# Kernel optimization log

Measured on AMD Instinct MI355X. Metric: run time of the kernel, lower is better.

Reference implementation:

```python
import jax, jax.numpy as jnp
import numpy as np

ALPHA, NCLUST, LAMBD, GAMMA = 0.6, 3, 0.1, 0.01
KMEANS_ITERS = 10


def _conv(x, w, b):
    y = jax.lax.conv_general_dilated(x, w, (1, 1), 'SAME',
                                     dimension_numbers=('NCHW', 'OIHW', 'NCHW'))
    return y + b[None, :, None, None]


def _pool2(x):
    B, C, H, W = x.shape
    return x.reshape(B, C, H // 2, 2, W // 2, 2).mean(axis=(3, 5))


def _up2(x):
    return jnp.repeat(jnp.repeat(x, 2, axis=2), 2, axis=3)


def _encode(x, p, all_features=False):
    f1 = jax.nn.relu(_conv(x, p['e1_w'], p['e1_b']))
    f2 = jax.nn.relu(_conv(_pool2(f1), p['e2_w'], p['e2_b']))
    f3 = jax.nn.relu(_conv(_pool2(f2), p['e3_w'], p['e3_b']))
    f4 = jax.nn.relu(_conv(_pool2(f3), p['e4_w'], p['e4_b']))
    return (f1, f2, f3, f4) if all_features else f4


def _decode(f, p):
    x = jax.nn.relu(_conv(f, p['d1_w'], p['d1_b']))
    x = jax.nn.relu(_conv(_up2(x), p['d2_w'], p['d2_b']))
    x = jax.nn.relu(_conv(_up2(x), p['d3_w'], p['d3_b']))
    return _conv(_up2(x), p['d4_w'], p['d4_b'])


def _kmeans_onehot(pts, k):
    # pts: [N, C]; fixed-iteration Lloyd's, init = first k points.
    cent0 = pts[:k]

    def step(cent, _):
        d = ((pts[:, None, :] - cent[None]) ** 2).sum(-1)  # [N, K]
        oh = jax.nn.one_hot(jnp.argmin(d, axis=1), k, dtype=pts.dtype)
        cent = (oh.T @ pts) / (oh.sum(0)[:, None] + 1e-6)
        return cent, None

    cent, _ = jax.lax.scan(step, cent0, None, length=KMEANS_ITERS)
    d = ((pts[:, None, :] - cent[None]) ** 2).sum(-1)
    return jax.nn.one_hot(jnp.argmin(d, axis=1), k, dtype=pts.dtype)  # [N, K]


def _style_transfer(fc, fs):
    # fc, fs: [C, H, W] single-sample encoded features (original runs this per-sample on CPU numpy).
    C, H, W = fc.shape
    f = fc.reshape(C, -1)  # [C, N]
    s = fs.reshape(C, -1)  # [C, M]
    oh_c = _kmeans_onehot(f.T, NCLUST)  # [N, K]
    oh_s = _kmeans_onehot(s.T, NCLUST)  # [M, K]
    eye = LAMBD * jnp.eye(C, dtype=f.dtype)

    def cluster_T(wc, ws):
        # weighted whitening-coloring transform for one cluster pair
        nc = wc.sum() + 1e-6
        ns = ws.sum() + 1e-6
        mu_c = (f * wc).sum(1) / nc
        mu_s = (s * ws).sum(1) / ns
        fc_ = f - mu_c[:, None]
        fs_ = s - mu_s[:, None]
        cov_c = (fc_ * wc) @ fc_.T / nc + eye
        cov_s = (fs_ * ws) @ fs_.T / ns + eye
        lc, Ec = jnp.linalg.eigh(cov_c)
        ls, Es = jnp.linalg.eigh(cov_s)
        Wm = (Ec * jnp.clip(lc, 1e-6) ** -0.5) @ Ec.T  # whiten
        Cm = (Es * jnp.clip(ls, 1e-6) ** 0.5) @ Es.T   # color
        return Cm @ Wm, mu_c, mu_s

    Ts, mucs, muss = jax.vmap(cluster_T, in_axes=(1, 1))(oh_c, oh_s)  # [K,C,C],[K,C],[K,C]
    tpts = (jnp.einsum('kcd,dn->kcn', Ts, f)
            - jnp.einsum('kcd,kd->kc', Ts, mucs)[:, :, None]
            + muss[:, :, None])  # [K, C, N]
    fcs = jnp.einsum('nk,kcn->cn', oh_c, tpts)  # select per-point cluster transform
    return (ALPHA * fcs + (1.0 - ALPHA) * f).reshape(C, H, W)


def _forward(content_images, style_images, p):
    cf = _encode(content_images, p)
    sf = _encode(style_images, p)
    # original detaches to numpy -> no grad through the transfer
    tf_ = jax.lax.stop_gradient(jax.vmap(_style_transfer)(cf, sf))
    dec = _decode(tf_, p)
    ef = _encode(dec, p)
    all_ef = _encode(dec, p, all_features=True)
    all_sf = _encode(style_images, p, all_features=True)
    closs = jnp.mean((ef - cf) ** 2)
    sloss = 0.0
    for fa, fb in zip(all_ef, all_sf):
        sloss = sloss + jnp.mean((fa.mean((2, 3)) - fb.mean((2, 3))) ** 2)
        sloss = sloss + jnp.mean((fa.std((2, 3)) - fb.std((2, 3))) ** 2)
    return closs + GAMMA * sloss


PARAM_SHAPES = dict(
    e1_w=(64, 3, 3, 3), e1_b=(64,), e2_w=(128, 64, 3, 3), e2_b=(128,),
    e3_w=(256, 128, 3, 3), e3_b=(256,), e4_w=(512, 256, 3, 3), e4_b=(512,),
    d1_w=(256, 512, 3, 3), d1_b=(256,), d2_w=(128, 256, 3, 3), d2_b=(128,),
    d3_w=(64, 128, 3, 3), d3_b=(64,), d4_w=(3, 64, 3, 3), d4_b=(3,),
)


def setup_inputs() -> dict:
    key = jax.random.key(0)
    kc, ks, kp = jax.random.split(key, 3)
    inp = {
        'content_images': jax.random.uniform(kc, (4, 3, 256, 256), jnp.float32),
        'style_images': jax.random.uniform(ks, (4, 3, 256, 256), jnp.float32),
    }
    for i, (name, shp) in enumerate(PARAM_SHAPES.items()):
        fan_in = int(np.prod(shp[1:])) if len(shp) > 1 else 1
        inp[name] = jax.random.normal(jax.random.fold_in(kp, i), shp, jnp.float32) / np.sqrt(fan_in)
    return inp


def reference(content_images, style_images, e1_w, e1_b, e2_w, e2_b, e3_w, e3_b,
              e4_w, e4_b, d1_w, d1_b, d2_w, d2_b, d3_w, d3_b, d4_w, d4_b):
    p = dict(e1_w=e1_w, e1_b=e1_b, e2_w=e2_w, e2_b=e2_b, e3_w=e3_w, e3_b=e3_b,
             e4_w=e4_w, e4_b=e4_b, d1_w=d1_w, d1_b=d1_b, d2_w=d2_w, d2_b=d2_b,
             d3_w=d3_w, d3_b=d3_b, d4_w=d4_w, d4_b=d4_b)
    return _forward(content_images, style_images, p)
```

## Files before the change

### kernel.cpp

```cpp
#include <hip/hip_runtime.h>
#include <cstddef>

#define NS_ITERS 8
#define MSZ 262144
#define PL  6291456
#define KSLOT 12312

typedef unsigned short u16;
typedef __attribute__((ext_vector_type(8))) short bf16x8;
typedef __attribute__((ext_vector_type(4))) float f32x4;
typedef __attribute__((ext_vector_type(4))) short u16x4;

__device__ inline u16 bf16_rne(float x){
  unsigned u = __float_as_uint(x);
  unsigned r = u + 0x7fffu + ((u>>16)&1u);
  return (u16)(r>>16);
}
__device__ inline float bf16f(u16 h){
  return __uint_as_float(((unsigned)h)<<16);
}

#define OFF_F4C   0ul
#define OFF_F4S   2097152ul
#define OFF_TF    4194304ul
// ... 217 lines not shown
      const int c = (gc<<3) + i;
      float v;
      if constexpr (POOL){
        const float* p = in + ((size_t)(b*C + c0+c)*(Ho*2) + ho*2)*(size_t)(Wo*2) + (size_t)wo*2;
        v = 0.25f*(p[0] + p[1] + p[2*Wo] + p[2*Wo+1]);
      } else {
        v = in[((size_t)(b*C + c0+c))*N + n];
      }
      u16 h = bf16_rne(v);
      tr[c][lnn] = (unsigned)h | ((unsigned)bf16_rne(v - bf16f(h)) << 16);
    }
  }
  __syncthreads();
  const int n2 = threadIdx.x >> 3, oct = threadIdx.x & 7;
  bf16x8 vh, vl;
  #pragma unroll
  for (int j=0;j<8;j++){
    unsigned u = tr[(oct<<3)+j][n2];
    vh[j] = (short)(u & 0xffffu);
    vl[j] = (short)(u >> 16);
  }
  size_t o = ((size_t)b*N + (n0 + n2))*(size_t)C + c0 + (oct<<3);
  *(bf16x8*)&oh[o] = vh;
  *(bf16x8*)&ol[o] = vl;
}

template<int KS, int RESIZE>
__global__ __launch_bounds__(256,4) void convm(
    const u16* __restrict__ xh, const u16* __restrict__ xl,
    const u16* __restrict__ wsh, const u16* __restrict__ wsl,
    const float* __restrict__ bias, float* __restrict__ out,
    int Cin, int Cout, int H, int W, int relu)
{
  const int tilesW = W >> 4;
  const int h0 = (blockIdx.x / tilesW) << 3;
  const int w0 = (blockIdx.x % tilesW) << 4;
  const int co0 = blockIdx.y << 6;
  const int b  = blockIdx.z / KS;
  const int ks = blockIdx.z % KS;
  const int NB = gridDim.z / KS;
  const int tid = threadIdx.x;
  const int wid = tid >> 6, lane = tid & 63;
  const int wm = wid >> 1, wn = wid & 1;
  const int quad = lane >> 4, ln = lane & 15;

  __shared__ __align__(16) u16 sXh[180*40], sXl[180*40];
  __shared__ __align__(16) u16 sWh[64*40],  sWl[64*40];

  f32x4 acc[2][4];
  #pragma unroll
  for (int i=0;i<2;i++)
    #pragma unroll
    for (int j=0;j<4;j++)
      #pragma unroll
      for (int e=0;e<4;e++) acc[i][j][e] = 0.f;

  const int wco = tid >> 2, wcg = (tid & 3) << 3;

  const int ciA = ks*(Cin/KS), ciB = ciA + Cin/KS;
  for (int ci0 = ciA; ci0 < ciB; ci0 += 32){
    for (int e = tid; e < 720; e += 256){
      const int px = e >> 2, sl = e & 3;
      const int pr = px / 18, pc = px - pr*18;
      const int ih = h0 + pr - 1, iw = w0 + pc - 1;
      bf16x8 vh, vl;
      #pragma unroll
      for (int j=0;j<8;j++){ vh[j] = 0; vl[j] = 0; }
      if ((unsigned)ih < (unsigned)H && (unsigned)iw < (unsigned)W){
        size_t o;
        if constexpr (RESIZE==0)
          o = ((size_t)(b*H + ih)*W + iw)*(size_t)Cin + (size_t)(ci0 + sl*8);
        else
          o = ((size_t)(b*(H>>1) + (ih>>1))*(W>>1) + (iw>>1))*(size_t)Cin + (size_t)(ci0 + sl*8);
        vh = *(const bf16x8*)&xh[o];
        vl = *(const bf16x8*)&xl[o];
      }
      *(bf16x8*)&sXh[px*40 + sl*8] = vh;
      *(bf16x8*)&sXl[px*40 + sl*8] = vl;
    }
    for (int dh = 0; dh < 3; ++dh){
      for (int dw = 0; dw < 3; ++dw){
        {
          const size_t so = ((size_t)((dh*3+dw)*Cout + co0+wco))*Cin + ci0 + wcg;
          *(bf16x8*)&sWh[wco*40 + wcg] = *(const bf16x8*)&wsh[so];
          *(bf16x8*)&sWl[wco*40 + wcg] = *(const bf16x8*)&wsl[so];
        }
        __syncthreads();
        bf16x8 ah[2], al[2], bh[4], bl[4];
        #pragma unroll
        for (int t=0;t<2;t++){
          const int co_l = (wm*2+t)*16 + ln;
          ah[t] = *(const bf16x8*)&sWh[co_l*40 + quad*8];
          al[t] = *(const bf16x8*)&sWl[co_l*40 + quad*8];
        }
        #pragma unroll
        for (int t=0;t<4;t++){
          const int p = (wn*4+t)*16 + ln;
          const int px = ((p>>4) + dh)*18 + (p&15) + dw;
          const int xo = px*40 + quad*8;
          bh[t] = *(const bf16x8*)&sXh[xo];
          bl[t] = *(const bf16x8*)&sXl[xo];
        }
        #pragma unroll
        for (int mi=0;mi<2;mi++)
          #pragma unroll
          for (int ni=0;ni<4;ni++){
            acc[mi][ni] = __builtin_amdgcn_mfma_f32_16x16x32_bf16(ah[mi], bh[ni], acc[mi][ni], 0, 0, 0);
            acc[mi][ni] = __builtin_amdgcn_mfma_f32_16x16x32_bf16(ah[mi], bl[ni], acc[mi][ni], 0, 0, 0);
            acc[mi][ni] = __builtin_amdgcn_mfma_f32_16x16x32_bf16(al[mi], bh[ni], acc[mi][ni], 0, 0, 0);
          }
        __syncthreads();
      }
    }
  }
  #pragma unroll
  for (int mi=0;mi<2;mi++){
    const int co = co0 + (wm*2+mi)*16 + quad*4;
    #pragma unroll
    for (int ni=0;ni<4;ni++){
      const int p = (wn*4+ni)*16 + ln;
      const int oh = h0 + (p>>4), ow = w0 + (p&15);
      #pragma unroll
      for (int rg=0; rg<4; rg++){
        const int cog = co + rg;
        if constexpr (KS==1){
          float v = acc[mi][ni][rg] + bias[cog];
          if (relu) v = fmaxf(v, 0.f);
          out[((size_t)(b*Cout + cog)*H + oh)*W + ow] = v;
        } else {
          out[((size_t)((ks*NB + b)*Cout + cog)*H + oh)*W + ow] = acc[mi][ni][rg];
        }
      }
    }
  }
}

__global__ __launch_bounds__(256) void sumk(const float* __restrict__ part, const float* __restrict__ bias,
                                            float* __restrict__ out, int Cout, int HW, int KS, int relu, int n){
  int idx = blockIdx.x*256 + threadIdx.x;
  if (idx >= n) return;
  int co = (idx / HW) % Cout;
  float v = bias[co];
  for (int k=0;k<KS;k++) v += part[(size_t)k*n + idx];
  if (relu) v = fmaxf(v, 0.f);
  out[idx] = v;
}

__global__ __launch_bounds__(256) void statsk(const float* __restrict__ x, int HW,
                                              float* __restrict__ mo, float* __restrict__ so){
  int bc = blockIdx.x, tid = threadIdx.x;
  const float* p = x + (size_t)bc*HW;
  double s = 0.0, s2 = 0.0;
  for (int i = tid; i < HW; i += 256){ double v = p[i]; s += v; s2 += v*v; }
  __shared__ double sh[256], sh2[256];
  sh[tid] = s; sh2[tid] = s2; __syncthreads();
  for (int k=128;k>0;k>>=1){ if (tid<k){ sh[tid]+=sh[tid+k]; sh2[tid]+=sh2[tid+k]; } __syncthreads(); }
  if (tid == 0){
    double m = sh[0]/HW;
    double var = sh2[0]/HW - m*m;
    if (var < 0.0) var = 0.0;
    mo[bc] = (float)m;
    so[bc] = (float)sqrt(var);
  }
}

__global__ __launch_bounds__(256) void transposek(const float* __restrict__ f4c,
                                                  const float* __restrict__ f4s,
                                                  float* __restrict__ ptsT){
  __shared__ float t[32][33];
  int r = blockIdx.z;
  const float* src = (r < 4) ? (f4c + (size_t)r*524288) : (f4s + (size_t)(r-4)*524288);
  int n0 = blockIdx.x*32, c0 = blockIdx.y*32;
  int lx = threadIdx.x & 31, ly = threadIdx.x >> 5;
  for (int j=0;j<32;j+=8)
    t[ly+j][lx] = src[(size_t)(c0+ly+j)*1024 + n0+lx];
  __syncthreads();
  for (int j=0;j<32;j+=8)
    ptsT[((size_t)r*1024 + n0+ly+j)*512 + c0+lx] = t[lx][ly+j];
}

__global__ __launch_bounds__(256) void initcent2k(const float* __restrict__ ptsT, float* __restrict__ KACC){
  int i = blockIdx.x*256 + threadIdx.x;
  if (i < 12288){
    int c = i & 511; int k = (i >> 9) % 3; int r = i / 1536;
    KACC[r*1536 + k*512 + c] = ptsT[((size_t)r*1024 + k)*512 + c];
  }
  if (i < 24) KACC[12288 + i] = 1.f;
}

__global__ __launch_bounds__(256) void kstepk(const float* __restrict__ ptsT,
    const float* __restrict__ prev, float* __restrict__ next,
    int* __restrict__ a, int nodiv)
{
  const int r = blockIdx.x, sl = blockIdx.y;
  const int tid = threadIdx.x;
  __shared__ float sc[1536];
  __shared__ int sa[32];
  __shared__ float red[3][8][32];
  __shared__ int scnt[3];
  if (tid < 3) scnt[tid] = 0;
  for (int i = tid; i < 1536; i += 256){
    float s = prev[r*1536 + i];
    float cnt = nodiv ? 1.f : (prev[12288 + r*3 + (i>>9)] + 1e-6f);
    sc[i] = s / cnt;
  }
  __syncthreads();
  const float* base = ptsT + (size_t)r*524288;
  const int wid = tid >> 6, lane = tid & 63;
  for (int rep = 0; rep < 8; ++rep){
    int p = wid*8 + rep;
    int n = sl*32 + p;
    const float* pp = base + (size_t)n*512;
    float d0=0.f,d1=0.f,d2=0.f;
    #pragma unroll
    for (int i=0;i<8;i++){
      int c = lane + i*64;
      float v = pp[c];
      float e0 = v - sc[c], e1 = v - sc[512+c], e2 = v - sc[1024+c];
      d0 = fmaf(e0,e0,d0); d1 = fmaf(e1,e1,d1); d2 = fmaf(e2,e2,d2);
    }
    #pragma unroll
    for (int off=32; off>0; off>>=1){
      d0 += __shfl_down(d0, off, 64);
      d1 += __shfl_down(d1, off, 64);
      d2 += __shfl_down(d2, off, 64);
    }
    if (lane == 0){
      int bi = 0; float bd = d0;
      if (d1 < bd){ bd = d1; bi = 1; }
      if (d2 < bd){ bd = d2; bi = 2; }
      sa[p] = bi;
      a[r*1024 + n] = bi;
    }
  }
  __syncthreads();
  if (tid < 32) atomicAdd(&scnt[sa[tid]], 1);
  __syncthreads();
  if (tid < 3) atomicAdd(&next[12288 + r*3 + tid], (float)scnt[tid]);
  const int g = tid >> 5, lc = tid & 31;
  for (int cj = 0; cj < 16; ++cj){
    int c = cj*32 + lc;
    float s0=0.f,s1=0.f,s2=0.f;
    #pragma unroll
    for (int q=0;q<4;q++){
      int nl = g*4 + q;
      float v = base[(size_t)(sl*32+nl)*512 + c];
      int an = sa[nl];
      s0 += (an==0)?v:0.f;
      s1 += (an==1)?v:0.f;
      s2 += (an==2)?v:0.f;
    }
    red[0][g][lc]=s0; red[1][g][lc]=s1; red[2][g][lc]=s2;
    __syncthreads();
    if (g == 0){
      float t0=0.f,t1=0.f,t2=0.f;
      #pragma unroll
      for (int q2=0;q2<8;q2++){ t0+=red[0][q2][lc]; t1+=red[1][q2][lc]; t2+=red[2][q2][lc]; }
      atomicAdd(&next[r*1536 +          c], t0);
      atomicAdd(&next[r*1536 +  512 +   c], t1);
      atomicAdd(&next[r*1536 + 1024 +   c], t2);
    }
    __syncthreads();
  }
}

__global__ __launch_bounds__(256) void mufink(const float* __restrict__ slot,
                                              float* __restrict__ mu, float* __restrict__ counts){
  int i = blockIdx.x*256 + threadIdx.x;
  if (i >= 12288) return;
  int c = i & 511; int k = (i >> 9) % 3; int r = i / 1536;
  int cs = r >> 2, img = r & 3;
  int i0 = cs*12 + img*3;
  float cnt = slot[12288 + r*3 + k];
  mu[(size_t)(i0+k)*512 + c] = slot[r*1536 + k*512 + c] / (cnt + 1e-6f);
  if (c == 0) counts[i0+k] = cnt;
}

__global__ __launch_bounds__(256) void maskcenterk(const float* __restrict__ f4c, const float* __restrict__ f4s,
        const int* __restrict__ a, const float* __restrict__ mu,
        u16* __restrict__ Ph, u16* __restrict__ Pl){
  size_t i4 = ((size_t)blockIdx.x*256 + threadIdx.x)*4;
  if (i4 >= (size_t)PL*2) return;
  int z = (int)(i4 >> 19);
  int rc = (int)(i4 & 524287);
  int c = rc >> 10, n = rc & 1023;
  int cs = z / 12; int rem = z - cs*12; int img = rem / 3; int k = rem - img*3;
  const float* pts = (cs ? f4s : f4c) + (size_t)img*524288;
  float m = mu[(size_t)z*512 + c];
  const int* an = a + (cs*4 + img)*1024 + n;
  float4 v4 = *(const float4*)&pts[(size_t)c*1024 + n];
  float vv[4] = {v4.x, v4.y, v4.z, v4.w};
  u16x4 oh, ol;
  #pragma unroll
  for (int j=0;j<4;j++){
    float v = (an[j] == k) ? (vv[j] - m) : 0.f;
    u16 h = bf16_rne(v);
    oh[j] = (short)h;
    ol[j] = (short)bf16_rne(v - bf16f(h));
  }
  *(u16x4*)&Ph[i4] = oh;
  *(u16x4*)&Pl[i4] = ol;
}

__global__ __launch_bounds__(256,4) void covgemm(const u16* __restrict__ Ph, const u16* __restrict__ Pl,
        const float* __restrict__ counts, float* __restrict__ Ycov, float* __restrict__ trsum){
  const int z = blockIdx.z;
  const u16* Pbh = Ph + (size_t)z*524288;
  const u16* Pbl = Pl + (size_t)z*524288;
  const int m0 = blockIdx.y*128, n0 = blockIdx.x*64;
  const int tid = threadIdx.x;

  __shared__ __align__(16) u16 sAh[128*40], sAl[128*40];
  __shared__ __align__(16) u16 sBh[64*40], sBl[64*40];

  const int ra = tid >> 2, qa = tid & 3;
  const int wid = tid >> 6, lane = tid & 63;
  const int wm = wid >> 1, wn = wid & 1;
  const int quad = lane >> 4, ln = lane & 15;

  f32x4 acc[4][2];
  #pragma unroll
  for (int i=0;i<4;i++)
    #pragma unroll
    for (int j=0;j<2;j++)
      #pragma unroll
      for (int e=0;e<4;e++) acc[i][j][e] = 0.f;

  for (int k0 = 0; k0 < 1024; k0 += 32){
    *(bf16x8*)&sAh[ra*40 + qa*8]      = *(const bf16x8*)&Pbh[(size_t)(m0+ra)*1024    + k0 + qa*8];
    *(bf16x8*)&sAl[ra*40 + qa*8]      = *(const bf16x8*)&Pbl[(size_t)(m0+ra)*1024    + k0 + qa*8];
    *(bf16x8*)&sAh[(ra+64)*40 + qa*8] = *(const bf16x8*)&Pbh[(size_t)(m0+ra+64)*1024 + k0 + qa*8];
    *(bf16x8*)&sAl[(ra+64)*40 + qa*8] = *(const bf16x8*)&Pbl[(size_t)(m0+ra+64)*1024 + k0 + qa*8];
    *(bf16x8*)&sBh[ra*40 + qa*8]      = *(const bf16x8*)&Pbh[(size_t)(n0+ra)*1024    + k0 + qa*8];
    *(bf16x8*)&sBl[ra*40 + qa*8]      = *(const bf16x8*)&Pbl[(size_t)(n0+ra)*1024    + k0 + qa*8];
    __syncthreads();

    bf16x8 ah[4], al[4], bh[2], bl[2];
    #pragma unroll
    for (int t=0;t<4;t++){
      const int moA = ((wm*4+t)*16 + ln)*40 + quad*8;
      ah[t] = *(const bf16x8*)&sAh[moA];
      al[t] = *(const bf16x8*)&sAl[moA];
    }
    #pragma unroll
    for (int t=0;t<2;t++){
      const int moB = ((wn*2+t)*16 + ln)*40 + quad*8;
      bh[t] = *(const bf16x8*)&sBh[moB];
      bl[t] = *(const bf16x8*)&sBl[moB];
    }
    #pragma unroll
    for (int mi=0;mi<4;mi++)
      #pragma unroll
      for (int ni=0;ni<2;ni++){
        acc[mi][ni] = __builtin_amdgcn_mfma_f32_16x16x32_bf16(ah[mi], bh[ni], acc[mi][ni], 0, 0, 0);
        acc[mi][ni] = __builtin_amdgcn_mfma_f32_16x16x32_bf16(ah[mi], bl[ni], acc[mi][ni], 0, 0, 0);
        acc[mi][ni] = __builtin_amdgcn_mfma_f32_16x16x32_bf16(al[mi], bh[ni], acc[mi][ni], 0, 0, 0);
      }
    __syncthreads();
  }
  const float inv = 1.f/(counts[z] + 1e-6f);
  float dsum = 0.f; bool anyd = false;
  #pragma unroll
  for (int mi=0;mi<4;mi++){
    const int mbase = m0 + (wm*4+mi)*16 + quad*4;
    #pragma unroll
    for (int ni=0;ni<2;ni++){
      const int n = n0 + (wn*2+ni)*16 + ln;
      #pragma unroll
      for (int rg=0;rg<4;rg++){
        const int m = mbase + rg;
        float v = acc[mi][ni][rg]*inv + ((m==n)?0.1f:0.f);
        Ycov[(size_t)z*MSZ + (size_t)m*512 + n] = v;
        if (m==n){ dsum += v; anyd = true; }
      }
    }
  }
  if (anyd) atomicAdd(&trsum[z], dsum);
}

__global__ __launch_bounds__(256) void nsinitk(const float* __restrict__ Ycov, const float* __restrict__ sval,
                                               u16* __restrict__ Yh, u16* __restrict__ Yl,
                                               u16* __restrict__ Zh, u16* __restrict__ Zl){
  size_t idx = (size_t)blockIdx.x*256 + threadIdx.x;
  if (idx >= (size_t)PL) return;
  int z = (int)(idx >> 18);
  int rc = (int)(idx & (MSZ-1));
  int rr = rc >> 9, cc = rc & 511;
  float y = Ycov[idx] / sval[z];
  u16 h = bf16_rne(y);
  Yh[idx] = h;
  Yl[idx] = bf16_rne(y - bf16f(h));
  Zh[idx] = (rr==cc) ? (u16)0x3F80 : (u16)0;
  Zl[idx] = 0;
}

template<int MODE>
__global__ __launch_bounds__(256,4) void bmms(
    const u16* __restrict__ Ah, const u16* __restrict__ Al,
    const u16* __restrict__ Bh, const u16* __restrict__ Bl,
    u16* __restrict__ Ch, u16* __restrict__ Cl,
    const float* __restrict__ osc,
    int aoff, float* __restrict__ trAcc)
{
  const int z = blockIdx.z;
  const u16* Abh = Ah + (size_t)(z+aoff)*MSZ;
  const u16* Abl = Al + (size_t)(z+aoff)*MSZ;
  const u16* Bbh = Bh + (size_t)z*MSZ;
  const u16* Bbl = Bl + (size_t)z*MSZ;
  const int m0 = blockIdx.y*128, n0 = blockIdx.x*64;
  const int tid = threadIdx.x;

  __shared__ __align__(16) u16 sAh[128*40], sAl[128*40];
  __shared__ __align__(16) u16 sBh[64*40], sBl[64*40];

  const int ra = tid >> 2, qa = tid & 3;
  const int wid = tid >> 6, lane = tid & 63;
  const int wm = wid >> 1, wn = wid & 1;
  const int quad = lane >> 4, ln = lane & 15;

  f32x4 acc[4][2];
  #pragma unroll
  for (int i=0;i<4;i++)
    #pragma unroll
    for (int j=0;j<2;j++)
      #pragma unroll
      for (int e=0;e<4;e++) acc[i][j][e] = 0.f;

  for (int k0 = 0; k0 < 512; k0 += 32){
    *(bf16x8*)&sAh[ra*40 + qa*8]      = *(const bf16x8*)&Abh[(size_t)(m0+ra)*512    + k0 + qa*8];
    *(bf16x8*)&sAl[ra*40 + qa*8]      = *(const bf16x8*)&Abl[(size_t)(m0+ra)*512    + k0 + qa*8];
    *(bf16x8*)&sAh[(ra+64)*40 + qa*8] = *(const bf16x8*)&Abh[(size_t)(m0+ra+64)*512 + k0 + qa*8];
    *(bf16x8*)&sAl[(ra+64)*40 + qa*8] = *(const bf16x8*)&Abl[(size_t)(m0+ra+64)*512 + k0 + qa*8];
    *(bf16x8*)&sBh[ra*40 + qa*8]      = *(const bf16x8*)&Bbh[(size_t)(n0+ra)*512    + k0 + qa*8];
    *(bf16x8*)&sBl[ra*40 + qa*8]      = *(const bf16x8*)&Bbl[(size_t)(n0+ra)*512    + k0 + qa*8];
    __syncthreads();

    bf16x8 ah[4], al[4], bh[2], bl[2];
    #pragma unroll
    for (int t=0;t<4;t++){
      const int moA = ((wm*4+t)*16 + ln)*40 + quad*8;
      ah[t] = *(const bf16x8*)&sAh[moA];
      al[t] = *(const bf16x8*)&sAl[moA];
    }
    #pragma unroll
    for (int t=0;t<2;t++){
      const int moB = ((wn*2+t)*16 + ln)*40 + quad*8;
      bh[t] = *(const bf16x8*)&sBh[moB];
      bl[t] = *(const bf16x8*)&sBl[moB];
    }
    #pragma unroll
    for (int mi=0;mi<4;mi++)
      #pragma unroll
      for (int ni=0;ni<2;ni++){
        acc[mi][ni] = __builtin_amdgcn_mfma_f32_16x16x32_bf16(ah[mi], bh[ni], acc[mi][ni], 0, 0, 0);
        acc[mi][ni] = __builtin_amdgcn_mfma_f32_16x16x32_bf16(ah[mi], bl[ni], acc[mi][ni], 0, 0, 0);
        acc[mi][ni] = __builtin_amdgcn_mfma_f32_16x16x32_bf16(al[mi], bh[ni], acc[mi][ni], 0, 0, 0);
      }
    __syncthreads();
  }

  float alpha = 1.f;
  if constexpr (MODE==2){ alpha = osc[z]; }

  float dsum = 0.f; bool anyd = false;
  #pragma unroll
  for (int mi=0;mi<4;mi++){
    const int mbase = m0 + (wm*4+mi)*16 + quad*4;
    #pragma unroll
    for (int ni=0;ni<2;ni++){
      const int n = n0 + (wn*2+ni)*16 + ln;
      #pragma unroll
      for (int rg=0;rg<4;rg++){
        const int m = mbase + rg;
        const size_t off = (size_t)z*MSZ + (size_t)m*512 + n;
        float v = alpha*acc[mi][ni][rg];
        u16 h = bf16_rne(v);
        Ch[off] = h;
        Cl[off] = bf16_rne(v - bf16f(h));
        if (MODE==0 && trAcc && m==n){ dsum += v; anyd = true; }
      }
    }
  }
  if (MODE==0 && anyd) atomicAdd(&trAcc[z], dsum);
}

__global__ __launch_bounds__(256) void bmmpair(
    const u16* __restrict__ Yh, const u16* __restrict__ Yl,
    const u16* __restrict__ Mh, const u16* __restrict__ Ml,
    const u16* __restrict__ Zh, const u16* __restrict__ Zl,
    u16* __restrict__ Y2h, u16* __restrict__ Y2l,
    u16* __restrict__ Z2h, u16* __restrict__ Z2l,
    const float* __restrict__ trAcc, int last)
{
  const int z = blockIdx.z;
  int zz; bool isY;
  if (last){ zz = z; isY = (z >= 12); }
  else { isY = (z < 24); zz = isY ? z : (z - 24); }
  const size_t zo = (size_t)zz*MSZ;
  const u16 *Abh, *Abl, *Bbh, *Bbl, *Dbh, *Dbl;
  u16 *Cbh, *Cbl;
  if (isY){
    Abh = Yh + zo; Abl = Yl + zo;
    Bbh = Mh + zo; Bbl = Ml + zo;
    Dbh = Yh + zo; Dbl = Yl + zo;
    Cbh = Y2h + zo; Cbl = Y2l + zo;
  } else {
    Abh = Mh + zo; Abl = Ml + zo;
    Bbh = Zh + zo; Bbl = Zl + zo;
    Dbh = Zh + zo; Dbl = Zl + zo;
    Cbh = Z2h + zo; Cbl = Z2l + zo;
  }
  const int m0 = blockIdx.y*128, n0 = blockIdx.x*128;
  const int tid = threadIdx.x;

  __shared__ __align__(16) u16 sAh[128*40], sAl[128*40];
  __shared__ __align__(16) u16 sBh[128*40], sBl[128*40];

  const int ra = tid >> 2, qa = tid & 3;
  const int wid = tid >> 6, lane = tid & 63;
  const int wm = wid >> 1, wn = wid & 1;
  const int quad = lane >> 4, ln = lane & 15;

  f32x4 acc[4][4];
  #pragma unroll
  for (int i=0;i<4;i++)
    #pragma unroll
    for (int j=0;j<4;j++)
      #pragma unroll
      for (int e=0;e<4;e++) acc[i][j][e] = 0.f;

  for (int k0 = 0; k0 < 512; k0 += 32){
    *(bf16x8*)&sAh[ra*40 + qa*8]      = *(const bf16x8*)&Abh[(size_t)(m0+ra)*512    + k0 + qa*8];
    *(bf16x8*)&sAl[ra*40 + qa*8]      = *(const bf16x8*)&Abl[(size_t)(m0+ra)*512    + k0 + qa*8];
    *(bf16x8*)&sAh[(ra+64)*40 + qa*8] = *(const bf16x8*)&Abh[(size_t)(m0+ra+64)*512 + k0 + qa*8];
    *(bf16x8*)&sAl[(ra+64)*40 + qa*8] = *(const bf16x8*)&Abl[(size_t)(m0+ra+64)*512 + k0 + qa*8];
    *(bf16x8*)&sBh[ra*40 + qa*8]      = *(const bf16x8*)&Bbh[(size_t)(n0+ra)*512    + k0 + qa*8];
    *(bf16x8*)&sBl[ra*40 + qa*8]      = *(const bf16x8*)&Bbl[(size_t)(n0+ra)*512    + k0 + qa*8];
    *(bf16x8*)&sBh[(ra+64)*40 + qa*8] = *(const bf16x8*)&Bbh[(size_t)(n0+ra+64)*512 + k0 + qa*8];
    *(bf16x8*)&sBl[(ra+64)*40 + qa*8] = *(const bf16x8*)&Bbl[(size_t)(n0+ra+64)*512 + k0 + qa*8];
    __syncthreads();

    bf16x8 ah[4], al[4], bh[4], bl[4];
    #pragma unroll
    for (int t=0;t<4;t++){
      const int moA = ((wm*4+t)*16 + ln)*40 + quad*8;
      const int moB = ((wn*4+t)*16 + ln)*40 + quad*8;
      ah[t] = *(const bf16x8*)&sAh[moA];
      al[t] = *(const bf16x8*)&sAl[moA];
      bh[t] = *(const bf16x8*)&sBh[moB];
      bl[t] = *(const bf16x8*)&sBl[moB];
    }
    #pragma unroll
    for (int mi=0;mi<4;mi++)
      #pragma unroll
      for (int ni=0;ni<4;ni++){
        acc[mi][ni] = __builtin_amdgcn_mfma_f32_16x16x32_bf16(ah[mi], bh[ni], acc[mi][ni], 0, 0, 0);
        acc[mi][ni] = __builtin_amdgcn_mfma_f32_16x16x32_bf16(ah[mi], bl[ni], acc[mi][ni], 0, 0, 0);
        acc[mi][ni] = __builtin_amdgcn_mfma_f32_16x16x32_bf16(al[mi], bh[ni], acc[mi][ni], 0, 0, 0);
      }
    __syncthreads();
  }

  const float tr = trAcc[zz];
  const float g2 = fminf(512.f/fmaxf(tr, 1e-6f), 2.7f);
  const float oz = 0.5f*sqrtf(g2);
  const float alpha = -g2*oz, beta = 3.f*oz;

  #pragma unroll
  for (int mi=0;mi<4;mi++){
    const int mbase = m0 + (wm*4+mi)*16 + quad*4;
    #pragma unroll
    for (int ni=0;ni<4;ni++){
      const int n = n0 + (wn*4+ni)*16 + ln;
      #pragma unroll
      for (int rg=0;rg<4;rg++){
        const int m = mbase + rg;
        const size_t off = (size_t)m*512 + n;
        float v = alpha*acc[mi][ni][rg] + beta*(bf16f(Dbh[off]) + bf16f(Dbl[off]));
        u16 h = bf16_rne(v);
        Cbh[off] = h;
        Cbl[off] = bf16_rne(v - bf16f(h));
      }
    }
  }
}

__global__ __launch_bounds__(256,4) void bmmt(
    const u16* __restrict__ Th, const u16* __restrict__ Tl,
    const u16* __restrict__ fh, const u16* __restrict__ fl,
    float* __restrict__ Cf)
{
  const int z = blockIdx.z;
  const u16* Abh = Th + (size_t)z*MSZ;
  const u16* Abl = Tl + (size_t)z*MSZ;
  const u16* Bbh = fh + (size_t)(z/3)*524288;
  const u16* Bbl = fl + (size_t)(z/3)*524288;
  const int m0 = blockIdx.y*128, n0 = blockIdx.x*64;
  const int tid = threadIdx.x;

  __shared__ __align__(16) u16 sAh[128*40], sAl[128*40];
  __shared__ __align__(16) u16 sBh[64*40], sBl[64*40];

  const int ra = tid >> 2, qa = tid & 3;
  const int wid = tid >> 6, lane = tid & 63;
  const int wm = wid >> 1, wn = wid & 1;
  const int quad = lane >> 4, ln = lane & 15;

  f32x4 acc[4][2];
  #pragma unroll
  for (int i=0;i<4;i++)
    #pragma unroll
    for (int j=0;j<2;j++)
      #pragma unroll
      for (int e=0;e<4;e++) acc[i][j][e] = 0.f;

  for (int k0 = 0; k0 < 512; k0 += 32){
    *(bf16x8*)&sAh[ra*40 + qa*8]      = *(const bf16x8*)&Abh[(size_t)(m0+ra)*512    + k0 + qa*8];
    *(bf16x8*)&sAl[ra*40 + qa*8]      = *(const bf16x8*)&Abl[(size_t)(m0+ra)*512    + k0 + qa*8];
    *(bf16x8*)&sAh[(ra+64)*40 + qa*8] = *(const bf16x8*)&Abh[(size_t)(m0+ra+64)*512 + k0 + qa*8];
    *(bf16x8*)&sAl[(ra+64)*40 + qa*8] = *(const bf16x8*)&Abl[(size_t)(m0+ra+64)*512 + k0 + qa*8];
    *(bf16x8*)&sBh[ra*40 + qa*8]      = *(const bf16x8*)&Bbh[(size_t)(n0+ra)*512    + k0 + qa*8];
    *(bf16x8*)&sBl[ra*40 + qa*8]      = *(const bf16x8*)&Bbl[(size_t)(n0+ra)*512    + k0 + qa*8];
    __syncthreads();

    bf16x8 ah[4], al[4], bh[2], bl[2];
    #pragma unroll
    for (int t=0;t<4;t++){
      const int moA = ((wm*4+t)*16 + ln)*40 + quad*8;
      ah[t] = *(const bf16x8*)&sAh[moA];
      al[t] = *(const bf16x8*)&sAl[moA];
    }
    #pragma unroll
    for (int t=0;t<2;t++){
      const int moB = ((wn*2+t)*16 + ln)*40 + quad*8;
      bh[t] = *(const bf16x8*)&sBh[moB];
      bl[t] = *(const bf16x8*)&sBl[moB];
    }
    #pragma unroll
    for (int mi=0;mi<4;mi++)
      #pragma unroll
      for (int ni=0;ni<2;ni++){
        acc[mi][ni] = __builtin_amdgcn_mfma_f32_16x16x32_bf16(ah[mi], bh[ni], acc[mi][ni], 0, 0, 0);
        acc[mi][ni] = __builtin_amdgcn_mfma_f32_16x16x32_bf16(ah[mi], bl[ni], acc[mi][ni], 0, 0, 0);
        acc[mi][ni] = __builtin_amdgcn_mfma_f32_16x16x32_bf16(al[mi], bh[ni], acc[mi][ni], 0, 0, 0);
      }
    __syncthreads();
  }
  #pragma unroll
  for (int mi=0;mi<4;mi++){
    const int mbase = m0 + (wm*4+mi)*16 + quad*4;
    #pragma unroll
    for (int ni=0;ni<2;ni++){
      const int n = n0 + (wn*2+ni)*16 + ln;
      #pragma unroll
      for (int rg=0;rg<4;rg++){
        const int m = mbase + rg;
        Cf[(size_t)z*524288 + (size_t)m*1024 + n] = acc[mi][ni][rg];
      }
    }
  }
}

__global__ void make_scalesk(const float* __restrict__ sval, float* __restrict__ scl){
  int i = threadIdx.x;
  if (i < 12) scl[i] = sqrtf(sval[12+i] / sval[i]);
}

__global__ __launch_bounds__(512) void tveck(const u16* __restrict__ Th, const u16* __restrict__ Tl,
                                             const float* __restrict__ mu, float* __restrict__ tvec){
  int b = blockIdx.x; int c = threadIdx.x;
  __shared__ float mc[512];
  mc[c] = mu[(size_t)b*512 + c];
  __syncthreads();
  const u16* Trh = Th + ((size_t)b*512 + c)*512;
  const u16* Trl = Tl + ((size_t)b*512 + c)*512;
  float s = 0.f;
  for (int d=0; d<512; d++) s = fmaf(bf16f(Trh[d]) + bf16f(Trl[d]), mc[d], s);
  tvec[b*512 + c] = mu[(size_t)(12+b)*512 + c] - s;
}

__global__ __launch_bounds__(256) void selectk(const float* __restrict__ tpts, const float* __restrict__ tvec,
        const int* __restrict__ a, const float* __restrict__ f4c, float* __restrict__ tf){
  size_t idx = (size_t)blockIdx.x*256 + threadIdx.x;
  if (idx >= 2097152ul) return;
  int n = (int)(idx & 1023);
  int c = (int)((idx >> 10) & 511);
  int img = (int)(idx >> 19);
  int k = a[img*1024 + n];
  int b = img*3 + k;
  float v = tpts[((size_t)b*512 + c)*1024 + n] + tvec[b*512 + c];
  tf[idx] = 0.6f*v + 0.4f*f4c[idx];
}

__global__ __launch_bounds__(256) void clossk(const float* __restrict__ x, const float* __restrict__ y,
                                              int n, float* __restrict__ acc){
  int tid = threadIdx.x;
  float s = 0.f;
  for (size_t i = (size_t)blockIdx.x*256 + tid; i < (size_t)n; i += (size_t)gridDim.x*256){
    float d = x[i] - y[i]; s = fmaf(d, d, s);
  }
  __shared__ float sh[256];
  sh[tid] = s; __syncthreads();
  for (int k=128;k>0;k>>=1){ if (tid<k) sh[tid]+=sh[tid+k]; __syncthreads(); }
  if (tid==0) atomicAdd(acc, sh[0]);
}

__global__ __launch_bounds__(256) void finalk(const float* __restrict__ sm, float* __restrict__ out){
  int tid = threadIdx.x;
  const int cnts[4] = {256,512,1024,2048};
  const int offs[4] = {0,256,768,1792};
  const float* mS = sm + SM_STATS_S;
  const float* sS = sm + SM_STATS_S + 3840;
  const float* mD = sm + SM_STATS_D;
  const float* sD = sm + SM_STATS_D + 3840;
  double sl = 0.0;
  for (int L=0; L<4; ++L){
    int cnt = cnts[L], off = offs[L];
    double inv = 1.0/cnt;
    for (int i=tid; i<cnt; i+=256){
      double dm = (double)mD[off+i] - (double)mS[off+i];
      double ds = (double)sD[off+i] - (double)sS[off+i];
      sl += (dm*dm + ds*ds)*inv;
    }
  }
  __shared__ double sh[256];
  sh[tid] = sl; __syncthreads();
  for (int k=128;k>0;k>>=1){ if (tid<k) sh[tid]+=sh[tid+k]; __syncthreads(); }
  if (tid==0){
    double closs = (double)sm[SM_CLOSS] / 2097152.0;
    out[0] = (float)(closs + 0.01*sh[0]);
  }
}


extern "C" void kernel_launch(void* const* d_in, const int* in_sizes, int n_in,
                              void* d_out, int out_size, void* d_ws, size_t ws_size,
                              hipStream_t stream)
{
  const float* content = (const float*)d_in[0];
  const float* style   = (const float*)d_in[1];
  const float* Wm[8]; const float* Bm[8];
  for (int i=0;i<8;i++){ Wm[i] = (const float*)d_in[2+2*i]; Bm[i] = (const float*)d_in[3+2*i]; }
  float* out = (float*)d_out;
  float* ws = (float*)d_ws;

  float* f4c  = ws + OFF_F4C;
  float* f4s  = ws + OFF_F4S;
  float* tf   = ws + OFF_TF;
  float* dec  = ws + OFF_DEC;
  float* sm   = ws + OFF_SMALL;
  float* AR   = ws + OFF_ARENA;
  int*   aPtr = (int*)(sm + SM_ASSIGN);
  float* mu   = sm + SM_MU;
  float* counts = sm + SM_COUNTS;
  float* sval = sm + SM_SVAL;
  float* scl  = sm + SM_SCALE;
  float* tvec = sm + SM_TVEC;
  float* trbuf = sm + SM_TR;

  u16* WB = (u16*)(ws + OFF_WSPL);
  u16 *w2h=WB+0,       *w2l=WB+73728;
  u16 *w3h=WB+147456,  *w3l=WB+442368;
  u16 *w4h=WB+737280,  *w4l=WB+1916928;
  u16 *v1h=WB+3096576, *v1l=WB+4276224;
  u16 *v2h=WB+5455872, *v2l=WB+5750784;
  u16 *v3h=WB+6045696, *v3l=WB+6119424;

  float* Ycov = AR;
  u16* Mh  = (u16*)(AR);
  u16* Ml  = (u16*)(AR + 3145728ul);
  u16* Yh  = (u16*)(AR + 6291456ul);
  u16* Yl  = (u16*)(AR + 9437184ul);
  u16* Zh  = (u16*)(AR + 12582912ul);
  u16* Zl  = (u16*)(AR + 15728640ul);
  u16* Y2h = (u16*)(AR + 18874368ul);
  u16* Y2l = (u16*)(AR + 22020096ul);
  u16* Z2h = (u16*)(AR + 25165824ul);
  u16* Z2l = (u16*)(AR + 28311552ul);
  u16* Ph  = (u16*)(AR + 18874368ul);
  u16* Pl  = (u16*)(AR + 25165824ul);
  float* ptsT = AR + 25165824ul;
  u16* Th  = (u16*)(AR + 18874368ul);
  u16* Tl  = (u16*)(AR + 20971520ul);
  u16* fsh = (u16*)(AR + 23068672ul);
  u16* fsl = (u16*)(AR + 24117248ul);
  float* KACC = AR + 0;

  u16* xP1h  = (u16*)(AR + 16777216ul);
  u16* xP1l  = (u16*)(AR + 20971520ul);
  u16* xF2ph = (u16*)(AR + 16777216ul);
  u16* xF2pl = (u16*)(AR + 18874368ul);
  u16* xF3ph = (u16*)(AR + 18874368ul);
  u16* xF3pl = (u16*)(AR + 19922944ul);
  u16* xTFh  = (u16*)(AR + 8388608ul);
  u16* xTFl  = (u16*)(AR + 9437184ul);
  u16* xX1h  = (u16*)(AR + 1048576ul);
  u16* xX1l  = (u16*)(AR + 1572864ul);
  u16* xX2h  = (u16*)(AR + 11534336ul);
  u16* xX2l  = (u16*)(AR + 12582912ul);
  u16* xP1dh = (u16*)(AR + 16777216ul);
  u16* xP1dl = (u16*)(AR + 18874368ul);
  u16* xF2dph= (u16*)(AR + 16777216ul);
  u16* xF2dpl= (u16*)(AR + 17825792ul);
  u16* xF3dph= (u16*)(AR + 16777216ul);
  u16* xF3dpl= (u16*)(AR + 17301504ul);

  zerok<<<512,256,0,stream>>>(sm, 131072);

  {
    auto wsp = [&](int li, u16* wh, u16* wl, int Co, int Ci){
      int n = 9*Co*Ci;
      wsplitk<<<(n+255)/256,256,0,stream>>>(Wm[li], wh, wl, Co, Ci);
    };
    wsp(1,w2h,w2l,128,64);
    wsp(2,w3h,w3l,256,128);
    wsp(3,w4h,w4l,512,256);
    wsp(4,v1h,v1l,256,512);
    wsp(5,v2h,v2l,128,256);
    wsp(6,v3h,v3l,64,128);
  }

  auto convMFMA = [&](const u16* xh, const u16* xl, int li, float* outp,
                      int B,int Ci,int Co,int H,int Wd,int relu,int KS,int RZ,float* part){
    const u16 *wh=nullptr,*wl=nullptr;
    switch(li){
      case 1: wh=w2h; wl=w2l; break;
      case 2: wh=w3h; wl=w3l; break;
      case 3: wh=w4h; wl=w4l; break;
      case 4: wh=v1h; wl=v1l; break;
      case 5: wh=v2h; wl=v2l; break;
      case 6: wh=v3h; wl=v3l; break;
    }
    int tiles = (H>>3)*(Wd>>4);
    if (KS==1){
      dim3 g(tiles,Co>>6,B);
      if (RZ==0) convm<1,0><<<g,256,0,stream>>>(xh,xl,wh,wl,Bm[li],outp,Ci,Co,H,Wd,relu);
      else       convm<1,2><<<g,256,0,stream>>>(xh,xl,wh,wl,Bm[li],outp,Ci,Co,H,Wd,relu);
    } else if (KS==2){
      dim3 g(tiles,Co>>6,B*2);
      if (RZ==0) convm<2,0><<<g,256,0,stream>>>(xh,xl,wh,wl,nullptr,part,Ci,Co,H,Wd,relu);
      else       convm<2,2><<<g,256,0,stream>>>(xh,xl,wh,wl,nullptr,part,Ci,Co,H,Wd,relu);
      int n = B*Co*H*Wd;
      sumk<<<(n+255)/256,256,0,stream>>>(part,Bm[li],outp,Co,H*Wd,2,relu,n);
    } else {
      dim3 g(tiles,Co>>6,B*4);
      convm<4,0><<<g,256,0,stream>>>(xh,xl,wh,wl,nullptr,part,Ci,Co,H,Wd,relu);
      int n = B*Co*H*Wd;
      sumk<<<(n+255)/256,256,0,stream>>>(part,Bm[li],outp,Co,H*Wd,4,relu,n);
    }
  };

  float* mS = sm + SM_STATS_S;
  float* sS = sm + SM_STATS_S + 3840;

  float* F1   = AR + 0;
  float* F2_8 = AR + 0;
  float* F3_8 = AR + 0;
  float* PART8 = AR + 10485760ul;

  {
    dim3 ge(64, 8, 4);
    conv3x3<8,4,1,0,0><<<ge,256,0,stream>>>(content,Wm[0],Bm[0],F1,xP1h,           xP1l,           4,3,64,256,256,1);
    conv3x3<8,4,1,1,0><<<ge,256,0,stream>>>(style,  Wm[0],Bm[0],F1,xP1h+4194304ul, xP1l+4194304ul, 4,3,64,256,256,1);
  }
  statsk<<<256,256,0,stream>>>(F1,65536, mS+0, sS+0);

  convMFMA(xP1h,xP1l, 1, F2_8, 8, 64,128,128,128,1,1,0,nullptr);
  statsk<<<512,256,0,stream>>>(F2_8 + 8388608ul, 16384, mS+256, sS+256);
  repackk<1><<<dim3(128,2,8),256,0,stream>>>(F2_8, xF2ph, xF2pl, 128,64,64);
  convMFMA(xF2ph,xF2pl, 2, F3_8, 8, 128,256,64,64,1,1,0,nullptr);
  statsk<<<1024,256,0,stream>>>(F3_8 + 4194304ul, 4096, mS+768, sS+768);
  repackk<1><<<dim3(32,4,8),256,0,stream>>>(F3_8, xF3ph, xF3pl, 256,32,32);
  convMFMA(xF3ph,xF3pl, 3, f4c, 8, 256,512,32,32,1,2,0,PART8);
  statsk<<<2048,256,0,stream>>>(f4s,1024, mS+1792, sS+1792);

  transposek<<<dim3(32,16,8),256,0,stream>>>(f4c,f4s,ptsT);
  zerok<<<(12*KSLOT+255)/256,256,0,stream>>>(KACC, 12*KSLOT);
  initcent2k<<<48,256,0,stream>>>(ptsT,KACC);
  for (int it=0; it<=10; ++it){
    kstepk<<<dim3(8,32),256,0,stream>>>(ptsT, KACC + (size_t)it*KSLOT, KACC + (size_t)(it+1)*KSLOT, aPtr, it==0 ? 1 : 0);
  }
  mufink<<<48,256,0,stream>>>(KACC + 11ul*KSLOT, mu, counts);

  maskcenterk<<<12288,256,0,stream>>>(f4c,f4s,aPtr,mu,Ph,Pl);
  covgemm<<<dim3(8,4,24),256,0,stream>>>(Ph,Pl,counts,Ycov,sval);
  nsinitk<<<24576,256,0,stream>>>(Ycov,sval,Yh,Yl,Zh,Zl);

  u16 *Ych=Yh,*Ycl=Yl,*Zch=Zh,*Zcl=Zl,*Yah=Y2h,*Yal=Y2l,*Zah=Z2h,*Zal=Z2l;
  for (int it=0; it<NS_ITERS; ++it){
    bmms<0><<<dim3(8,4,24),256,0,stream>>>(Zch,Zcl,Ych,Ycl,Mh,Ml,nullptr,0,trbuf+it*24);
    if (it < NS_ITERS-1)
      bmmpair<<<dim3(4,4,48),256,0,stream>>>(Ych,Ycl,Mh,Ml,Zch,Zcl,Yah,Yal,Zah,Zal,trbuf+it*24,0);
    else
      bmmpair<<<dim3(4,4,24),256,0,stream>>>(Ych,Ycl,Mh,Ml,Zch,Zcl,Yah,Yal,Zah,Zal,trbuf+it*24,1);
    u16* t;
    t=Ych;Ych=Yah;Yah=t; t=Ycl;Ycl=Yal;Yal=t;
    t=Zch;Zch=Zah;Zah=t; t=Zcl;Zcl=Zal;Zal=t;
  }
  make_scalesk<<<1,64,0,stream>>>(sval,scl);
  bmms<2><<<dim3(8,4,12),256,0,stream>>>(Ych,Ycl,Zch,Zcl,Th,Tl,scl,12,nullptr);
  tveck<<<12,512,0,stream>>>(Th,Tl,mu,tvec);
  repackk<0><<<dim3(32,8,4),256,0,stream>>>(f4c, fsh, fsl, 512,32,32);
  float* Mb = AR + 0;
  bmmt<<<dim3(16,4,12),256,0,stream>>>(Th,Tl,fsh,fsl,Mb);
  selectk<<<8192,256,0,stream>>>(Mb,tvec,aPtr,f4c,tf);

  float* X1 = AR + 0;
  float* X2 = AR + 5242880ul;
  float* X3 = AR + 0;
  float* PARTA = AR + 2097152ul;
  float* PARTB = AR + 7340032ul;
  repackk<0><<<dim3(32,8,4),256,0,stream>>>(tf, xTFh, xTFl, 512,32,32);
  convMFMA(xTFh,xTFl, 4, X1, 4, 512,256,32,32,1,4,0,PARTA);
  repackk<0><<<dim3(32,4,4),256,0,stream>>>(X1, xX1h, xX1l, 256,32,32);
  convMFMA(xX1h,xX1l, 5, X2, 4, 256,128,64,64,1,2,2,PARTB);
  repackk<0><<<dim3(128,2,4),256,0,stream>>>(X2, xX2h, xX2l, 128,64,64);
  convMFMA(xX2h,xX2l, 6, X3, 4, 128,64,128,128,1,1,2,nullptr);
  d4upk<<<dim3(256,1,4),256,0,stream>>>(X3, Wm[7], Bm[7], dec);

  float* mD = sm + SM_STATS_D;
  float* sD = sm + SM_STATS_D + 3840;
  float* F1d = AR + 0;
  float* F2d = AR + 0;
  float* F3d = AR + 10485760ul;
  {
    dim3 ge(64, 8, 4);
    conv3x3<8,4,1,1,0><<<ge,256,0,stream>>>(dec,Wm[0],Bm[0],F1d,xP1dh,xP1dl,4,3,64,256,256,1);
  }
  statsk<<<256,256,0,stream>>>(F1d,65536, mD+0, sD+0);
  convMFMA(xP1dh,xP1dl, 1, F2d, 4, 64,128,128,128,1,1,0,nullptr);
  statsk<<<512,256,0,stream>>>(F2d,16384, mD+256, sD+256);
  repackk<1><<<dim3(128,2,4),256,0,stream>>>(F2d, xF2dph, xF2dpl, 128,64,64);
  convMFMA(xF2dph,xF2dpl, 2, F3d, 4, 128,256,64,64,1,1,0,nullptr);
  statsk<<<1024,256,0,stream>>>(F3d,4096, mD+768, sD+768);
  repackk<1><<<dim3(32,4,4),256,0,stream>>>(F3d, xF3dph, xF3dpl, 256,32,32);
  convMFMA(xF3dph,xF3dpl, 3, tf, 4, 256,512,32,32,1,2,0,PARTA);
  statsk<<<2048,256,0,stream>>>(tf,1024, mD+1792, sD+1792);
  clossk<<<2048,256,0,stream>>>(tf,f4c,2097152, sm+SM_CLOSS);
  finalk<<<1,256,0,stream>>>(sm,out);
}
```

Before: 2.378 ms.

## Widen covariance/NS GEMM tiles to 128x128 and skip identity-Z first Newton-Schulz matmul

The covgemm and bmms kernels now use 128x128 output tiles with a 4x4 MFMA accumulator per wave, which halves the grid and increases reuse of each staged A tile. The trace-accumulation guard is restricted to diagonal tiles. The first Newton-Schulz iteration no longer runs a GEMM with Z equal to the identity. It copies Y into M, computes the trace directly, and forms the new Z elementwise with three small kernels. The changes trade occupancy (launch bounds relaxed, more registers) and fewer blocks on the GPU for fewer redundant loads and one skipped batched matmul.

```diff
diff --git a/kernel.cpp b/kernel.cpp
--- a/kernel.cpp
+++ b/kernel.cpp
@@ -543,27 +543,27 @@
   *(u16x4*)&Pl[i4] = ol;
 }
 
-__global__ __launch_bounds__(256,4) void covgemm(const u16* __restrict__ Ph, const u16* __restrict__ Pl,
+__global__ __launch_bounds__(256) void covgemm(const u16* __restrict__ Ph, const u16* __restrict__ Pl,
         const float* __restrict__ counts, float* __restrict__ Ycov, float* __restrict__ trsum){
   const int z = blockIdx.z;
   const u16* Pbh = Ph + (size_t)z*524288;
   const u16* Pbl = Pl + (size_t)z*524288;
-  const int m0 = blockIdx.y*128, n0 = blockIdx.x*64;
+  const int m0 = blockIdx.y*128, n0 = blockIdx.x*128;
   const int tid = threadIdx.x;
 
   __shared__ __align__(16) u16 sAh[128*40], sAl[128*40];
-  __shared__ __align__(16) u16 sBh[64*40], sBl[64*40];
+  __shared__ __align__(16) u16 sBh[128*40], sBl[128*40];
 
   const int ra = tid >> 2, qa = tid & 3;
   const int wid = tid >> 6, lane = tid & 63;
   const int wm = wid >> 1, wn = wid & 1;
   const int quad = lane >> 4, ln = lane & 15;
 
-  f32x4 acc[4][2];
+  f32x4 acc[4][4];
   #pragma unroll
   for (int i=0;i<4;i++)
     #pragma unroll
-    for (int j=0;j<2;j++)
+    for (int j=0;j<4;j++)
       #pragma unroll
       for (int e=0;e<4;e++) acc[i][j][e] = 0.f;
 
@@ -574,25 +574,24 @@
     *(bf16x8*)&sAl[(ra+64)*40 + qa*8] = *(const bf16x8*)&Pbl[(size_t)(m0+ra+64)*1024 + k0 + qa*8];
     *(bf16x8*)&sBh[ra*40 + qa*8]      = *(const bf16x8*)&Pbh[(size_t)(n0+ra)*1024    + k0 + qa*8];
     *(bf16x8*)&sBl[ra*40 + qa*8]      = *(const bf16x8*)&Pbl[(size_t)(n0+ra)*1024    + k0 + qa*8];
+    *(bf16x8*)&sBh[(ra+64)*40 + qa*8] = *(const bf16x8*)&Pbh[(size_t)(n0+ra+64)*1024 + k0 + qa*8];
+    *(bf16x8*)&sBl[(ra+64)*40 + qa*8] = *(const bf16x8*)&Pbl[(size_t)(n0+ra+64)*1024 + k0 + qa*8];
     __syncthreads();
 
-    bf16x8 ah[4], al[4], bh[2], bl[2];
+    bf16x8 ah[4], al[4], bh[4], bl[4];
     #pragma unroll
     for (int t=0;t<4;t++){
       const int moA = ((wm*4+t)*16 + ln)*40 + quad*8;
+      const int moB = ((wn*4+t)*16 + ln)*40 + quad*8;
       ah[t] = *(const bf16x8*)&sAh[moA];
       al[t] = *(const bf16x8*)&sAl[moA];
-    }
-    #pragma unroll
-    for (int t=0;t<2;t++){
-      const int moB = ((wn*2+t)*16 + ln)*40 + quad*8;
       bh[t] = *(const bf16x8*)&sBh[moB];
       bl[t] = *(const bf16x8*)&sBl[moB];
     }
     #pragma unroll
     for (int mi=0;mi<4;mi++)
       #pragma unroll
-      for (int ni=0;ni<2;ni++){
+      for (int ni=0;ni<4;ni++){
         acc[mi][ni] = __builtin_amdgcn_mfma_f32_16x16x32_bf16(ah[mi], bh[ni], acc[mi][ni], 0, 0, 0);
         acc[mi][ni] = __builtin_amdgcn_mfma_f32_16x16x32_bf16(ah[mi], bl[ni], acc[mi][ni], 0, 0, 0);
         acc[mi][ni] = __builtin_amdgcn_mfma_f32_16x16x32_bf16(al[mi], bh[ni], acc[mi][ni], 0, 0, 0);
@@ -605,14 +604,14 @@
   for (int mi=0;mi<4;mi++){
     const int mbase = m0 + (wm*4+mi)*16 + quad*4;
     #pragma unroll
-    for (int ni=0;ni<2;ni++){
-      const int n = n0 + (wn*2+ni)*16 + ln;
+    for (int ni=0;ni<4;ni++){
+      const int n = n0 + (wn*4+ni)*16 + ln;
       #pragma unroll
       for (int rg=0;rg<4;rg++){
         const int m = mbase + rg;
         float v = acc[mi][ni][rg]*inv + ((m==n)?0.1f:0.f);
         Ycov[(size_t)z*MSZ + (size_t)m*512 + n] = v;
-        if (m==n){ dsum += v; anyd = true; }
+        if (m0==n0 && m==n){ dsum += v; anyd = true; }
       }
     }
   }
@@ -635,8 +634,68 @@
   Zl[idx] = 0;
 }
 
+__global__ __launch_bounds__(256) void nsm0k(const u16* __restrict__ Yh, const u16* __restrict__ Yl,
+                                             u16* __restrict__ Mh, u16* __restrict__ Ml){
+  size_t i4 = ((size_t)blockIdx.x*256 + threadIdx.x)*4;
+  if (i4 >= (size_t)PL) return;
+  u16x4 hv = *(const u16x4*)&Yh[i4];
+  u16x4 lv = *(const u16x4*)&Yl[i4];
+  u16x4 oh, ol;
+  #pragma unroll
+  for (int j=0;j<4;j++){
+    float v = bf16f((u16)hv[j]) + bf16f((u16)lv[j]);
+    u16 h = bf16_rne(v);
+    oh[j] = (short)h;
+    ol[j] = (short)bf16_rne(v - bf16f(h));
+  }
+  *(u16x4*)&Mh[i4] = oh;
+  *(u16x4*)&Ml[i4] = ol;
+}
+
+__global__ __launch_bounds__(256) void nstr0k(const u16* __restrict__ Yh, const u16* __restrict__ Yl,
+                                              float* __restrict__ tr){
+  int z = blockIdx.x, tid = threadIdx.x;
+  float s = 0.f;
+  for (int i = tid; i < 512; i += 256){
+    size_t o = (size_t)z*MSZ + (size_t)i*513;
+    s += bf16f(Yh[o]) + bf16f(Yl[o]);
+  }
+  __shared__ float sh[256];
+  sh[tid] = s; __syncthreads();
+  for (int k=128;k>0;k>>=1){ if (tid<k) sh[tid]+=sh[tid+k]; __syncthreads(); }
+  if (tid == 0) tr[z] = sh[0];
+}
+
+__global__ __launch_bounds__(256) void nsz0k(const u16* __restrict__ Mh, const u16* __restrict__ Ml,
+                                             u16* __restrict__ Z2h, u16* __restrict__ Z2l,
+                                             const float* __restrict__ trAcc){
+  size_t i4 = ((size_t)blockIdx.x*256 + threadIdx.x)*4;
+  if (i4 >= (size_t)PL) return;
+  int z = (int)(i4 >> 18);
+  int rc = (int)(i4 & (MSZ-1));
+  int row = rc >> 9, col = rc & 511;
+  const float tr = trAcc[z];
+  const float g2 = fminf(512.f/fmaxf(tr, 1e-6f), 2.7f);
+  const float oz = 0.5f*sqrtf(g2);
+  const float alpha = -g2*oz, beta = 3.f*oz;
+  u16x4 hv = *(const u16x4*)&Mh[i4];
+  u16x4 lv = *(const u16x4*)&Ml[i4];
+  u16x4 oh, ol;
+  #pragma unroll
+  for (int j=0;j<4;j++){
+    float m = bf16f((u16)hv[j]) + bf16f((u16)lv[j]);
+    float zv = (row == col + j) ? 1.f : 0.f;
+    float v = alpha*m + beta*zv;
+    u16 h = bf16_rne(v);
+    oh[j] = (short)h;
+    ol[j] = (short)bf16_rne(v - bf16f(h));
+  }
+  *(u16x4*)&Z2h[i4] = oh;
+  *(u16x4*)&Z2l[i4] = ol;
+}
+
 template<int MODE>
-__global__ __launch_bounds__(256,4) void bmms(
+__global__ __launch_bounds__(256) void bmms(
     const u16* __restrict__ Ah, const u16* __restrict__ Al,
     const u16* __restrict__ Bh, const u16* __restrict__ Bl,
     u16* __restrict__ Ch, u16* __restrict__ Cl,
@@ -648,22 +707,22 @@
   const u16* Abl = Al + (size_t)(z+aoff)*MSZ;
   const u16* Bbh = Bh + (size_t)z*MSZ;
   const u16* Bbl = Bl + (size_t)z*MSZ;
-  const int m0 = blockIdx.y*128, n0 = blockIdx.x*64;
+  const int m0 = blockIdx.y*128, n0 = blockIdx.x*128;
   const int tid = threadIdx.x;
 
   __shared__ __align__(16) u16 sAh[128*40], sAl[128*40];
-  __shared__ __align__(16) u16 sBh[64*40], sBl[64*40];
+  __shared__ __align__(16) u16 sBh[128*40], sBl[128*40];
 
   const int ra = tid >> 2, qa = tid & 3;
   const int wid = tid >> 6, lane = tid & 63;
   const int wm = wid >> 1, wn = wid & 1;
   const int quad = lane >> 4, ln = lane & 15;
 
-  f32x4 acc[4][2];
+  f32x4 acc[4][4];
   #pragma unroll
   for (int i=0;i<4;i++)
     #pragma unroll
-    for (int j=0;j<2;j++)
+    for (int j=0;j<4;j++)
       #pragma unroll
       for (int e=0;e<4;e++) acc[i][j][e] = 0.f;
 
@@ -674,25 +733,24 @@
     *(bf16x8*)&sAl[(ra+64)*40 + qa*8] = *(const bf16x8*)&Abl[(size_t)(m0+ra+64)*512 + k0 + qa*8];
     *(bf16x8*)&sBh[ra*40 + qa*8]      = *(const bf16x8*)&Bbh[(size_t)(n0+ra)*512    + k0 + qa*8];
     *(bf16x8*)&sBl[ra*40 + qa*8]      = *(const bf16x8*)&Bbl[(size_t)(n0+ra)*512    + k0 + qa*8];
+    *(bf16x8*)&sBh[(ra+64)*40 + qa*8] = *(const bf16x8*)&Bbh[(size_t)(n0+ra+64)*512 + k0 + qa*8];
+    *(bf16x8*)&sBl[(ra+64)*40 + qa*8] = *(const bf16x8*)&Bbl[(size_t)(n0+ra+64)*512 + k0 + qa*8];
     __syncthreads();
 
-    bf16x8 ah[4], al[4], bh[2], bl[2];
+    bf16x8 ah[4], al[4], bh[4], bl[4];
     #pragma unroll
     for (int t=0;t<4;t++){
       const int moA = ((wm*4+t)*16 + ln)*40 + quad*8;
+      const int moB = ((wn*4+t)*16 + ln)*40 + quad*8;
       ah[t] = *(const bf16x8*)&sAh[moA];
       al[t] = *(const bf16x8*)&sAl[moA];
-    }
-    #pragma unroll
-    for (int t=0;t<2;t++){
-      const int moB = ((wn*2+t)*16 + ln)*40 + quad*8;
       bh[t] = *(const bf16x8*)&sBh[moB];
       bl[t] = *(const bf16x8*)&sBl[moB];
     }
     #pragma unroll
     for (int mi=0;mi<4;mi++)
       #pragma unroll
-      for (int ni=0;ni<2;ni++){
+      for (int ni=0;ni<4;ni++){
         acc[mi][ni] = __builtin_amdgcn_mfma_f32_16x16x32_bf16(ah[mi], bh[ni], acc[mi][ni], 0, 0, 0);
         acc[mi][ni] = __builtin_amdgcn_mfma_f32_16x16x32_bf16(ah[mi], bl[ni], acc[mi][ni], 0, 0, 0);
         acc[mi][ni] = __builtin_amdgcn_mfma_f32_16x16x32_bf16(al[mi], bh[ni], acc[mi][ni], 0, 0, 0);
@@ -708,8 +766,8 @@
   for (int mi=0;mi<4;mi++){
     const int mbase = m0 + (wm*4+mi)*16 + quad*4;
     #pragma unroll
-    for (int ni=0;ni<2;ni++){
-      const int n = n0 + (wn*2+ni)*16 + ln;
+    for (int ni=0;ni<4;ni++){
+      const int n = n0 + (wn*4+ni)*16 + ln;
       #pragma unroll
       for (int rg=0;rg<4;rg++){
         const int m = mbase + rg;
@@ -718,7 +776,7 @@
         u16 h = bf16_rne(v);
         Ch[off] = h;
         Cl[off] = bf16_rne(v - bf16f(h));
-        if (MODE==0 && trAcc && m==n){ dsum += v; anyd = true; }
+        if (MODE==0 && trAcc && m0==n0 && m==n){ dsum += v; anyd = true; }
       }
     }
   }
@@ -1124,22 +1182,29 @@
   mufink<<<48,256,0,stream>>>(KACC + 11ul*KSLOT, mu, counts);
 
   maskcenterk<<<12288,256,0,stream>>>(f4c,f4s,aPtr,mu,Ph,Pl);
-  covgemm<<<dim3(8,4,24),256,0,stream>>>(Ph,Pl,counts,Ycov,sval);
+  covgemm<<<dim3(4,4,24),256,0,stream>>>(Ph,Pl,counts,Ycov,sval);
   nsinitk<<<24576,256,0,stream>>>(Ycov,sval,Yh,Yl,Zh,Zl);
 
   u16 *Ych=Yh,*Ycl=Yl,*Zch=Zh,*Zcl=Zl,*Yah=Y2h,*Yal=Y2l,*Zah=Z2h,*Zal=Z2l;
   for (int it=0; it<NS_ITERS; ++it){
-    bmms<0><<<dim3(8,4,24),256,0,stream>>>(Zch,Zcl,Ych,Ycl,Mh,Ml,nullptr,0,trbuf+it*24);
-    if (it < NS_ITERS-1)
-      bmmpair<<<dim3(4,4,48),256,0,stream>>>(Ych,Ycl,Mh,Ml,Zch,Zcl,Yah,Yal,Zah,Zal,trbuf+it*24,0);
-    else
-      bmmpair<<<dim3(4,4,24),256,0,stream>>>(Ych,Ycl,Mh,Ml,Zch,Zcl,Yah,Yal,Zah,Zal,trbuf+it*24,1);
+    if (it == 0){
+      nsm0k<<<6144,256,0,stream>>>(Ych,Ycl,Mh,Ml);
+      nstr0k<<<24,256,0,stream>>>(Ych,Ycl,trbuf);
+      bmmpair<<<dim3(4,4,24),256,0,stream>>>(Ych,Ycl,Mh,Ml,Zch,Zcl,Yah,Yal,Zah,Zal,trbuf,0);
+      nsz0k<<<6144,256,0,stream>>>(Mh,Ml,Zah,Zal,trbuf);
+    } else {
+      bmms<0><<<dim3(4,4,24),256,0,stream>>>(Zch,Zcl,Ych,Ycl,Mh,Ml,nullptr,0,trbuf+it*24);
+      if (it < NS_ITERS-1)
+        bmmpair<<<dim3(4,4,48),256,0,stream>>>(Ych,Ycl,Mh,Ml,Zch,Zcl,Yah,Yal,Zah,Zal,trbuf+it*24,0);
+      else
+        bmmpair<<<dim3(4,4,24),256,0,stream>>>(Ych,Ycl,Mh,Ml,Zch,Zcl,Yah,Yal,Zah,Zal,trbuf+it*24,1);
+    }
     u16* t;
     t=Ych;Ych=Yah;Yah=t; t=Ycl;Ycl=Yal;Yal=t;
     t=Zch;Zch=Zah;Zah=t; t=Zcl;Zcl=Zal;Zal=t;
   }
   make_scalesk<<<1,64,0,stream>>>(sval,scl);
-  bmms<2><<<dim3(8,4,12),256,0,stream>>>(Ych,Ycl,Zch,Zcl,Th,Tl,scl,12,nullptr);
+  bmms<2><<<dim3(4,4,12),256,0,stream>>>(Ych,Ycl,Zch,Zcl,Th,Tl,scl,12,nullptr);
   tveck<<<12,512,0,stream>>>(Th,Tl,mu,tvec);
   repackk<0><<<dim3(32,8,4),256,0,stream>>>(f4c, fsh, fsl, 512,32,32);
   float* Mb = AR + 0;
```

After: 2.227 ms. 1.07x faster.
